# Kernel tuning notes

Hardware: AMD Instinct MI355X
Metric: run time of the kernel (lower is better)

## Reference

```python
import jax, jax.numpy as jnp
import numpy as np

N_NODES = 100000


def gcn_conv(x, src, dst, W, b):
    """PyG GCNConv: h = x @ W; A_hat = D^-1/2 (A + I) D^-1/2; out = A_hat h + b."""
    n = x.shape[0]
    h = x @ W                                           # [N, d_out]
    # degree with self-loops: deg_i = 1 + (# incoming edges to i)
    deg = jnp.ones((n,), x.dtype).at[dst].add(jnp.ones_like(dst, x.dtype))
    dinv = jax.lax.rsqrt(deg)                           # deg >= 1 always
    norm = dinv[src] * dinv[dst]                        # [E]
    msg = h[src] * norm[:, None]                        # [E, d_out] gather
    agg = jax.ops.segment_sum(msg, dst, num_segments=n)  # scatter-add
    agg = agg + h * (dinv * dinv)[:, None]              # self-loop term
    return agg + b


def setup_inputs() -> dict:
    key = jax.random.key(0)
    k1, k2, k3, k4, k5, k6 = jax.random.split(key, 6)
    in_dim, hid, out_dim = 256, 128, 40
    n_edges = 1600000
    x = jax.random.normal(k1, (N_NODES, in_dim), jnp.float32)
    edge_index = jax.random.randint(k2, (2, n_edges), 0, N_NODES, jnp.int64)
    # Glorot init like PyG GCNConv, zero bias
    W1 = jax.random.normal(k3, (in_dim, hid), jnp.float32) * np.sqrt(2.0 / (in_dim + hid))
    b1 = jnp.zeros((hid,), jnp.float32)
    W2 = jax.random.normal(k4, (hid, out_dim), jnp.float32) * np.sqrt(2.0 / (hid + out_dim))
    b2 = jnp.zeros((out_dim,), jnp.float32)
    return {"x": x, "edge_index": edge_index, "W1": W1, "b1": b1, "W2": W2, "b2": b2}


def reference(x, edge_index, W1, b1, W2, b2):
    src, dst = edge_index[0], edge_index[1]
    h = gcn_conv(x, src, dst, W1, b1)
    h = jax.nn.relu(h)
    # dropout is identity in eval mode (reference baseline)
    logits = gcn_conv(h, src, dst, W2, b2)
    return logits
```

## Files before the change

### kernel.cpp

```cpp
#include <hip/hip_runtime.h>

#define N_NODES 100000
#define N_EDGES 1600000

typedef unsigned int u32;
typedef unsigned short u16;
typedef __attribute__((ext_vector_type(8))) short bf16x8;
typedef __attribute__((ext_vector_type(4))) float f32x4;

__device__ __forceinline__ u16 f2b(float f) {
  u32 u = __builtin_bit_cast(u32, f);
  u32 r = (u + 0x7FFFu + ((u >> 16) & 1u)) >> 16;
  return (u16)r;
}
__device__ __forceinline__ float b2f(u32 bits) {
  return __builtin_bit_cast(float, bits << 16);
}
__device__ __forceinline__ u32 pack2(float x, float y) {
  return (u32)f2b(x) | ((u32)f2b(y) << 16);
}

__global__ __launch_bounds__(256) void hist_kernel(
    const int* __restrict__ dst, int* __restrict__ degcnt, int E) {
  int i = blockIdx.x * blockDim.x + threadIdx.x;
  int stride = gridDim.x * blockDim.x;
  for (; i < E; i += stride) atomicAdd(&degcnt[dst[i]], 1);
}

__global__ __launch_bounds__(256) void dinv_kernel(
    const int* __restrict__ degcnt, float* __restrict__ dinv, int n) {
  int i = blockIdx.x * blockDim.x + threadIdx.x;
  if (i < n) dinv[i] = rsqrtf(1.0f + (float)degcnt[i]);
}

__global__ __launch_bounds__(256) void scan1_kernel(
    const int* __restrict__ deg, int* __restrict__ rowstart, int* __restrict__ bsum, int n) {
  __shared__ int lds[256];
  int base = blockIdx.x * 512;
  int t = threadIdx.x;
  int i0 = base + t * 2, i1 = i0 + 1;
  int a = (i0 < n) ? deg[i0] : 0;
  int b = (i1 < n) ? deg[i1] : 0;
  int pairsum = a + b;
  lds[t] = pairsum;
  __syncthreads();
#pragma unroll
  for (int off = 1; off < 256; off <<= 1) {
    int v = lds[t];
    int add = (t >= off) ? lds[t - off] : 0;
    __syncthreads();
    lds[t] = v + add;
    __syncthreads();
  }
  int prev = (t > 0) ? lds[t - 1] : 0;
  if (i0 < n) rowstart[i0 + 1] = prev + a;
  if (i1 < n) rowstart[i1 + 1] = prev + pairsum;
  if (t == 255) bsum[blockIdx.x] = lds[255];
}

__global__ __launch_bounds__(256) void scan2_kernel(int* __restrict__ bsum, int nb) {
  __shared__ int lds[256];
  int t = threadIdx.x;
  lds[t] = (t < nb) ? bsum[t] : 0;
  __syncthreads();
#pragma unroll
  for (int off = 1; off < 256; off <<= 1) {
    int v = lds[t];
    int add = (t >= off) ? lds[t - off] : 0;
    __syncthreads();
    lds[t] = v + add;
    __syncthreads();
  }
  if (t < nb) bsum[t] = (t > 0) ? lds[t - 1] : 0;
}

__global__ __launch_bounds__(256) void scan3_kernel(
    int* __restrict__ rowstart, const int* __restrict__ bsum, int n) {
  int i = blockIdx.x * blockDim.x + threadIdx.x;
  if (i < n) rowstart[i + 1] += bsum[i >> 9];
  if (i == 0) rowstart[0] = 0;
}

__global__ __launch_bounds__(256) void fill_kernel(
    const int* __restrict__ src, const int* __restrict__ dst,
    const float* __restrict__ dinv, const int* __restrict__ rowstart,
    int* __restrict__ cursor, int* __restrict__ csr_src, float* __restrict__ csr_norm, int E) {
  int i = blockIdx.x * blockDim.x + threadIdx.x;
  int stride = gridDim.x * blockDim.x;
  for (; i < E; i += stride) {
    int s = src[i], d = dst[i];
    int pos = rowstart[d] + atomicAdd(&cursor[d], 1);
    csr_src[pos] = s;
    csr_norm[pos] = dinv[s] * dinv[d];
  }
}

__global__ __launch_bounds__(256) void cast_w1_kernel(
    const float* __restrict__ W, u16* __restrict__ Bt) {
  int i = blockIdx.x * 256 + threadIdx.x;
  int c = i & 127, k = i >> 7;
  Bt[c * 256 + k] = f2b(W[k * 128 + c]);
}
__global__ __launch_bounds__(256) void cast_w2_kernel(
    const float* __restrict__ W, u16* __restrict__ Bt) {
  int i = blockIdx.x * 256 + threadIdx.x;
  int c = i >> 7, k = i & 127;
  float v = (c < 40) ? W[k * 40 + c] : 0.f;
  Bt[c * 128 + k] = f2b(v);
}

__global__ __launch_bounds__(256) void gemm1_kernel(
    const float* __restrict__ A, const u16* __restrict__ Bt,
    u16* __restrict__ Cb, int M) {
  __shared__ __align__(16) u16 As[64 * 40];
  __shared__ __align__(16) u16 Bs[128 * 40];
  const int tid = threadIdx.x;
  const int row0 = blockIdx.x * 64;
  const int w = tid >> 6, l = tid & 63;
  const int lr = l & 15, lk = l >> 4;
  f32x4 acc[8];
#pragma unroll
  for (int n = 0; n < 8; ++n) acc[n] = (f32x4){0.f, 0.f, 0.f, 0.f};

  const int arow = tid >> 2;
  const int akq = (tid & 3) * 8;
  const int ag = min(row0 + arow, M - 1);
  const float* ap0 = A + (size_t)ag * 256 + akq;
  const int bcol = tid >> 1;
  const int bko = (tid & 1) * 16;
  const u16* bp0 = Bt + (size_t)bcol * 256 + bko;

  for (int kt = 0; kt < 256; kt += 32) {
    float4 v0 = *(const float4*)(ap0 + kt);
    float4 v1 = *(const float4*)(ap0 + kt + 4);
    uint4 ac;
    ac.x = pack2(v0.x, v0.y);
    ac.y = pack2(v0.z, v0.w);
    ac.z = pack2(v1.x, v1.y);
    ac.w = pack2(v1.z, v1.w);
    *(uint4*)(&As[arow * 40 + akq]) = ac;
    const uint4* bp = (const uint4*)(bp0 + kt);
    uint4 b0 = bp[0];
    uint4 b1 = bp[1];
    *(uint4*)(&Bs[bcol * 40 + bko]) = b0;
    *(uint4*)(&Bs[bcol * 40 + bko + 8]) = b1;
    __syncthreads();
    bf16x8 af = *(const bf16x8*)(&As[(w * 16 + lr) * 40 + lk * 8]);
#pragma unroll
    for (int n = 0; n < 8; ++n) {
      bf16x8 bf = *(const bf16x8*)(&Bs[(n * 16 + lr) * 40 + lk * 8]);
      acc[n] = __builtin_amdgcn_mfma_f32_16x16x32_bf16(af, bf, acc[n], 0, 0, 0);
    }
    __syncthreads();
  }
  const int orow = row0 + w * 16 + (l >> 4) * 4;
#pragma unroll
  for (int n = 0; n < 8; ++n) {
#pragma unroll
    for (int i = 0; i < 4; ++i) {
      int r = orow + i;
      if (r < M) Cb[(size_t)r * 128 + n * 16 + lr] = f2b(acc[n][i]);
    }
  }
}

__global__ __launch_bounds__(256) void gather1_kernel(
    const int* __restrict__ rowstart, const int* __restrict__ csr_src,
    const float* __restrict__ csr_norm, const float* __restrict__ dinv,
    const u16* __restrict__ hb, const float* __restrict__ bias,
    u16* __restrict__ outb, int n) {
  int w = (blockIdx.x * blockDim.x + threadIdx.x) >> 6;
  int lane = threadIdx.x & 63;
  if (w >= n) return;
  int beg = rowstart[w], end = rowstart[w + 1];
  int q = lane >> 4;
  int cq = (lane & 15) * 8;
  float a0[8], a1[8];
#pragma unroll
  for (int j = 0; j < 8; ++j) { a0[j] = 0.f; a1[j] = 0.f; }
  for (int e0 = beg; e0 < end; e0 += 8) {
    int ea = e0 + q;
    int eb = e0 + 4 + q;
    int ca = min(ea, end - 1);
    int cb = min(eb, end - 1);
    float na = (ea < end) ? csr_norm[ca] : 0.f;
    float nb = (eb < end) ? csr_norm[cb] : 0.f;
    int sa = csr_src[ca];
    int sb = csr_src[cb];
    uint4 va = *(const uint4*)(hb + (size_t)sa * 128 + cq);
    uint4 vb = *(const uint4*)(hb + (size_t)sb * 128 + cq);
    const u32* pa = (const u32*)&va;
    const u32* pb = (const u32*)&vb;
#pragma unroll
    for (int j = 0; j < 4; ++j) {
      a0[2 * j]     += b2f(pa[j] & 0xffffu) * na;
      a0[2 * j + 1] += b2f(pa[j] >> 16) * na;
      a1[2 * j]     += b2f(pb[j] & 0xffffu) * nb;
      a1[2 * j + 1] += b2f(pb[j] >> 16) * nb;
    }
  }
#pragma unroll
  for (int j = 0; j < 8; ++j) a0[j] += a1[j];
#pragma unroll
  for (int off = 16; off < 64; off <<= 1) {
#pragma unroll
    for (int j = 0; j < 8; ++j) a0[j] += __shfl_xor(a0[j], off);
  }
  if (q == 0) {
    float di = dinv[w];
    float sl = di * di;
    uint4 hv = *(const uint4*)(hb + (size_t)w * 128 + cq);
    const u32* ph = (const u32*)&hv;
    float4 b0 = *(const float4*)(bias + cq);
    float4 b1v = *(const float4*)(bias + cq + 4);
    float bb[8] = {b0.x, b0.y, b0.z, b0.w, b1v.x, b1v.y, b1v.z, b1v.w};
    float r[8];
#pragma unroll
    for (int j = 0; j < 4; ++j) {
      r[2 * j]     = fmaxf(a0[2 * j]     + b2f(ph[j] & 0xffffu) * sl + bb[2 * j], 0.f);
      r[2 * j + 1] = fmaxf(a0[2 * j + 1] + b2f(ph[j] >> 16)     * sl + bb[2 * j + 1], 0.f);
    }
    uint4 o;
    o.x = pack2(r[0], r[1]);
    o.y = pack2(r[2], r[3]);
    o.z = pack2(r[4], r[5]);
    o.w = pack2(r[6], r[7]);
    *(uint4*)(outb + (size_t)w * 128 + cq) = o;
  }
}

__global__ __launch_bounds__(256) void gemm2_kernel(
    const u16* __restrict__ Ab, const u16* __restrict__ Bt,
    u16* __restrict__ Cb, int M) {
  __shared__ __align__(16) u16 Bs[48 * 136];
  const int tid = threadIdx.x;
  const int row0 = blockIdx.x * 64;
  const int w = tid >> 6, l = tid & 63;
  const int lr = l & 15, lk = l >> 4;
#pragma unroll
  for (int i = 0; i < 3; ++i) {
    int ch = tid + i * 256;
    int col = ch >> 4;
    int ko = (ch & 15) * 8;
    *(uint4*)(&Bs[col * 136 + ko]) = *(const uint4*)(Bt + col * 128 + ko);
  }
  __syncthreads();
  f32x4 acc[3];
#pragma unroll
  for (int n = 0; n < 3; ++n) acc[n] = (f32x4){0.f, 0.f, 0.f, 0.f};
  const int arow = min(row0 + w * 16 + lr, M - 1);
  const u16* ap = Ab + (size_t)arow * 128 + lk * 8;
#pragma unroll
  for (int kt = 0; kt < 4; ++kt) {
    bf16x8 af = *(const bf16x8*)(ap + kt * 32);
#pragma unroll
    for (int n = 0; n < 3; ++n) {
      bf16x8 bf = *(const bf16x8*)(&Bs[(n * 16 + lr) * 136 + kt * 32 + lk * 8]);
      acc[n] = __builtin_amdgcn_mfma_f32_16x16x32_bf16(af, bf, acc[n], 0, 0, 0);
    }
  }
  const int orow = row0 + w * 16 + (l >> 4) * 4;
#pragma unroll
  for (int n = 0; n < 3; ++n) {
    int c = n * 16 + lr;
    if (c < 40) {
#pragma unroll
      for (int i = 0; i < 4; ++i) {
        int r = orow + i;
        if (r < M) Cb[(size_t)r * 40 + c] = f2b(acc[n][i]);
      }
    }
  }
}

__global__ __launch_bounds__(256) void gather2_kernel(
    const int* __restrict__ rowstart, const int* __restrict__ csr_src,
    const float* __restrict__ csr_norm, const float* __restrict__ dinv,
    const u16* __restrict__ hb, const float* __restrict__ bias,
    float* __restrict__ out, int n) {
  int w = (blockIdx.x * blockDim.x + threadIdx.x) >> 6;
  int lane = threadIdx.x & 63;
  if (w >= n || lane >= 40) return;
  int beg = rowstart[w], end = rowstart[w + 1];
  float acc0 = 0.f, acc1 = 0.f, acc2 = 0.f, acc3 = 0.f;
  for (int e0 = beg; e0 < end; e0 += 4) {
    int c1 = min(e0 + 1, end - 1);
    int c2 = min(e0 + 2, end - 1);
    int c3 = min(e0 + 3, end - 1);
    float n0 = csr_norm[e0];
    float n1 = (e0 + 1 < end) ? csr_norm[c1] : 0.f;
    float n2 = (e0 + 2 < end) ? csr_norm[c2] : 0.f;
    float n3 = (e0 + 3 < end) ? csr_norm[c3] : 0.f;
    int s0 = csr_src[e0], s1 = csr_src[c1], s2 = csr_src[c2], s3 = csr_src[c3];
    acc0 += b2f(hb[(size_t)s0 * 40 + lane]) * n0;
    acc1 += b2f(hb[(size_t)s1 * 40 + lane]) * n1;
    acc2 += b2f(hb[(size_t)s2 * 40 + lane]) * n2;
    acc3 += b2f(hb[(size_t)s3 * 40 + lane]) * n3;
  }
  float di = dinv[w];
  out[(size_t)w * 40 + lane] =
      (acc0 + acc1) + (acc2 + acc3) + b2f(hb[(size_t)w * 40 + lane]) * di * di + bias[lane];
}

extern "C" void kernel_launch(void* const* d_in, const int* in_sizes, int n_in,
                              void* d_out, int out_size, void* d_ws, size_t ws_size,
                              hipStream_t stream) {
  const float* x  = (const float*)d_in[0];
  const int*  ei  = (const int*)d_in[1];
  const float* W1 = (const float*)d_in[2];
  const float* b1 = (const float*)d_in[3];
  const float* W2 = (const float*)d_in[4];
  const float* b2 = (const float*)d_in[5];
  const int* src = ei;
  const int* dst = ei + N_EDGES;
  float* out = (float*)d_out;

  char* ws = (char*)d_ws;
  int*   degcnt   = (int*)(ws);
  float* dinv     = (float*)(ws + 400384);
  int*   rowstart = (int*)(ws + 800768);
  int*   bsum     = (int*)(ws + 1202176);
  int*   csr_src  = (int*)(ws + 1203200);
  float* csr_norm = (float*)(ws + 7603200);
  u16*   w1t      = (u16*)(ws + 14003200);
  u16*   w2t      = (u16*)(ws + 14068736);
  u16*   h1b      = (u16*)(ws + 14081024);
  u16*   agg1b    = (u16*)(ws + 39681024);
  u16*   h2b      = (u16*)(ws + 65281024);

  cast_w1_kernel<<<128, 256, 0, stream>>>(W1, w1t);
  cast_w2_kernel<<<24, 256, 0, stream>>>(W2, w2t);

  hipMemsetAsync(degcnt, 0, N_NODES * sizeof(int), stream);
  hist_kernel<<<2048, 256, 0, stream>>>(dst, degcnt, N_EDGES);
  dinv_kernel<<<(N_NODES + 255) / 256, 256, 0, stream>>>(degcnt, dinv, N_NODES);
  scan1_kernel<<<196, 256, 0, stream>>>(degcnt, rowstart, bsum, N_NODES);
  scan2_kernel<<<1, 256, 0, stream>>>(bsum, 196);
  scan3_kernel<<<(N_NODES + 255) / 256, 256, 0, stream>>>(rowstart, bsum, N_NODES);
  hipMemsetAsync(degcnt, 0, N_NODES * sizeof(int), stream);
  fill_kernel<<<2048, 256, 0, stream>>>(src, dst, dinv, rowstart, degcnt, csr_src, csr_norm, N_EDGES);

  gemm1_kernel<<<(N_NODES + 63) / 64, 256, 0, stream>>>(x, w1t, h1b, N_NODES);
  gather1_kernel<<<25000, 256, 0, stream>>>(rowstart, csr_src, csr_norm, dinv, h1b, b1, agg1b, N_NODES);

  gemm2_kernel<<<(N_NODES + 63) / 64, 256, 0, stream>>>(agg1b, w2t, h2b, N_NODES);
  gather2_kernel<<<25000, 256, 0, stream>>>(rowstart, csr_src, csr_norm, dinv, h2b, b2, out, N_NODES);
}
```

Before: 506.4 us.

## Record atomic rank during histogram and interleave CSR src/norm into int2

The histogram kernel now stores each edge's atomic return value as its rank within the destination row. The fill pass then computes the CSR position without a second atomic pass, which also drops the second memset. CSR source indices and normalisation weights are packed into one int2 array, so the gather kernels fetch both with a single 8-byte load. The rank buffer reuses the h2b workspace region and adds a 6.4 MB write in the histogram and a read in the fill pass.

Measured after the change: 456.3 us. 9.9% less time.

```diff
diff --git a/kernel.cpp b/kernel.cpp
--- a/kernel.cpp
+++ b/kernel.cpp
@@ -20,11 +20,11 @@
   return (u32)f2b(x) | ((u32)f2b(y) << 16);
 }
 
-__global__ __launch_bounds__(256) void hist_kernel(
-    const int* __restrict__ dst, int* __restrict__ degcnt, int E) {
+__global__ __launch_bounds__(256) void hist_rank_kernel(
+    const int* __restrict__ dst, int* __restrict__ degcnt, int* __restrict__ rank, int E) {
   int i = blockIdx.x * blockDim.x + threadIdx.x;
   int stride = gridDim.x * blockDim.x;
-  for (; i < E; i += stride) atomicAdd(&degcnt[dst[i]], 1);
+  for (; i < E; i += stride) rank[i] = atomicAdd(&degcnt[dst[i]], 1);
 }
 
 __global__ __launch_bounds__(256) void dinv_kernel(
@@ -81,17 +81,17 @@
   if (i == 0) rowstart[0] = 0;
 }
 
-__global__ __launch_bounds__(256) void fill_kernel(
+__global__ __launch_bounds__(256) void scatter_fill_kernel(
     const int* __restrict__ src, const int* __restrict__ dst,
-    const float* __restrict__ dinv, const int* __restrict__ rowstart,
-    int* __restrict__ cursor, int* __restrict__ csr_src, float* __restrict__ csr_norm, int E) {
+    const int* __restrict__ rank, const float* __restrict__ dinv,
+    const int* __restrict__ rowstart, int2* __restrict__ csr, int E) {
   int i = blockIdx.x * blockDim.x + threadIdx.x;
   int stride = gridDim.x * blockDim.x;
   for (; i < E; i += stride) {
     int s = src[i], d = dst[i];
-    int pos = rowstart[d] + atomicAdd(&cursor[d], 1);
-    csr_src[pos] = s;
-    csr_norm[pos] = dinv[s] * dinv[d];
+    float norm = dinv[s] * dinv[d];
+    int pos = rowstart[d] + rank[i];
+    csr[pos] = make_int2(s, __builtin_bit_cast(int, norm));
   }
 }
 
@@ -165,8 +165,8 @@
 }
 
 __global__ __launch_bounds__(256) void gather1_kernel(
-    const int* __restrict__ rowstart, const int* __restrict__ csr_src,
-    const float* __restrict__ csr_norm, const float* __restrict__ dinv,
+    const int* __restrict__ rowstart, const int2* __restrict__ csr,
+    const float* __restrict__ dinv,
     const u16* __restrict__ hb, const float* __restrict__ bias,
     u16* __restrict__ outb, int n) {
   int w = (blockIdx.x * blockDim.x + threadIdx.x) >> 6;
@@ -183,10 +183,12 @@
     int eb = e0 + 4 + q;
     int ca = min(ea, end - 1);
     int cb = min(eb, end - 1);
-    float na = (ea < end) ? csr_norm[ca] : 0.f;
-    float nb = (eb < end) ? csr_norm[cb] : 0.f;
-    int sa = csr_src[ca];
-    int sb = csr_src[cb];
+    int2 ta = csr[ca];
+    int2 tb = csr[cb];
+    float na = (ea < end) ? __builtin_bit_cast(float, ta.y) : 0.f;
+    float nb = (eb < end) ? __builtin_bit_cast(float, tb.y) : 0.f;
+    int sa = ta.x;
+    int sb = tb.x;
     uint4 va = *(const uint4*)(hb + (size_t)sa * 128 + cq);
     uint4 vb = *(const uint4*)(hb + (size_t)sb * 128 + cq);
     const u32* pa = (const u32*)&va;
@@ -274,8 +276,8 @@
 }
 
 __global__ __launch_bounds__(256) void gather2_kernel(
-    const int* __restrict__ rowstart, const int* __restrict__ csr_src,
-    const float* __restrict__ csr_norm, const float* __restrict__ dinv,
+    const int* __restrict__ rowstart, const int2* __restrict__ csr,
+    const float* __restrict__ dinv,
     const u16* __restrict__ hb, const float* __restrict__ bias,
     float* __restrict__ out, int n) {
   int w = (blockIdx.x * blockDim.x + threadIdx.x) >> 6;
@@ -287,15 +289,18 @@
     int c1 = min(e0 + 1, end - 1);
     int c2 = min(e0 + 2, end - 1);
     int c3 = min(e0 + 3, end - 1);
-    float n0 = csr_norm[e0];
-    float n1 = (e0 + 1 < end) ? csr_norm[c1] : 0.f;
-    float n2 = (e0 + 2 < end) ? csr_norm[c2] : 0.f;
-    float n3 = (e0 + 3 < end) ? csr_norm[c3] : 0.f;
-    int s0 = csr_src[e0], s1 = csr_src[c1], s2 = csr_src[c2], s3 = csr_src[c3];
-    acc0 += b2f(hb[(size_t)s0 * 40 + lane]) * n0;
-    acc1 += b2f(hb[(size_t)s1 * 40 + lane]) * n1;
-    acc2 += b2f(hb[(size_t)s2 * 40 + lane]) * n2;
-    acc3 += b2f(hb[(size_t)s3 * 40 + lane]) * n3;
+    int2 t0 = csr[e0];
+    int2 t1 = csr[c1];
+    int2 t2 = csr[c2];
+    int2 t3 = csr[c3];
+    float n0 = __builtin_bit_cast(float, t0.y);
+    float n1 = (e0 + 1 < end) ? __builtin_bit_cast(float, t1.y) : 0.f;
+    float n2 = (e0 + 2 < end) ? __builtin_bit_cast(float, t2.y) : 0.f;
+    float n3 = (e0 + 3 < end) ? __builtin_bit_cast(float, t3.y) : 0.f;
+    acc0 += b2f(hb[(size_t)t0.x * 40 + lane]) * n0;
+    acc1 += b2f(hb[(size_t)t1.x * 40 + lane]) * n1;
+    acc2 += b2f(hb[(size_t)t2.x * 40 + lane]) * n2;
+    acc3 += b2f(hb[(size_t)t3.x * 40 + lane]) * n3;
   }
   float di = dinv[w];
   out[(size_t)w * 40 + lane] =
@@ -320,29 +325,28 @@
   float* dinv     = (float*)(ws + 400384);
   int*   rowstart = (int*)(ws + 800768);
   int*   bsum     = (int*)(ws + 1202176);
-  int*   csr_src  = (int*)(ws + 1203200);
-  float* csr_norm = (float*)(ws + 7603200);
+  int2*  csr      = (int2*)(ws + 1203200);
   u16*   w1t      = (u16*)(ws + 14003200);
   u16*   w2t      = (u16*)(ws + 14068736);
   u16*   h1b      = (u16*)(ws + 14081024);
   u16*   agg1b    = (u16*)(ws + 39681024);
   u16*   h2b      = (u16*)(ws + 65281024);
+  int*   rank     = (int*)(ws + 65281024);
 
   cast_w1_kernel<<<128, 256, 0, stream>>>(W1, w1t);
   cast_w2_kernel<<<24, 256, 0, stream>>>(W2, w2t);
 
   hipMemsetAsync(degcnt, 0, N_NODES * sizeof(int), stream);
-  hist_kernel<<<2048, 256, 0, stream>>>(dst, degcnt, N_EDGES);
+  hist_rank_kernel<<<2048, 256, 0, stream>>>(dst, degcnt, rank, N_EDGES);
   dinv_kernel<<<(N_NODES + 255) / 256, 256, 0, stream>>>(degcnt, dinv, N_NODES);
   scan1_kernel<<<196, 256, 0, stream>>>(degcnt, rowstart, bsum, N_NODES);
   scan2_kernel<<<1, 256, 0, stream>>>(bsum, 196);
   scan3_kernel<<<(N_NODES + 255) / 256, 256, 0, stream>>>(rowstart, bsum, N_NODES);
-  hipMemsetAsync(degcnt, 0, N_NODES * sizeof(int), stream);
-  fill_kernel<<<2048, 256, 0, stream>>>(src, dst, dinv, rowstart, degcnt, csr_src, csr_norm, N_EDGES);
+  scatter_fill_kernel<<<2048, 256, 0, stream>>>(src, dst, rank, dinv, rowstart, csr, N_EDGES);
 
   gemm1_kernel<<<(N_NODES + 63) / 64, 256, 0, stream>>>(x, w1t, h1b, N_NODES);
-  gather1_kernel<<<25000, 256, 0, stream>>>(rowstart, csr_src, csr_norm, dinv, h1b, b1, agg1b, N_NODES);
+  gather1_kernel<<<25000, 256, 0, stream>>>(rowstart, csr, dinv, h1b, b1, agg1b, N_NODES);
 
   gemm2_kernel<<<(N_NODES + 63) / 64, 256, 0, stream>>>(agg1b, w2t, h2b, N_NODES);
-  gather2_kernel<<<25000, 256, 0, stream>>>(rowstart, csr_src, csr_norm, dinv, h2b, b2, out, N_NODES);
-}
+  gather2_kernel<<<25000, 256, 0, stream>>>(rowstart, csr, dinv, h2b, b2, out, N_NODES);
+}
```
